# Kernel optimization log

Hardware: AMD Instinct MI355X
Metric: run time of the kernel (lower is better)

The kernel has to match this reference:

```python
import jax, jax.numpy as jnp
import numpy as np

DIM = 2048
HEADS = 16
B = 2
T = 2048


def setup_inputs() -> dict:
    key = jax.random.key(0)
    k_x, k_qkv, k_out, k_b = jax.random.split(key, 4)
    inv = DIM ** -0.5
    return {
        "x": jax.random.normal(k_x, (B, T, DIM), dtype=jnp.float32),
        "w_qkv": jax.random.normal(k_qkv, (DIM, 3 * DIM), dtype=jnp.float32) * inv,
        "w_out": jax.random.normal(k_out, (DIM, DIM), dtype=jnp.float32) * inv,
        "b_out": jnp.zeros((DIM,), dtype=jnp.float32),
    }


def reference(x, w_qkv, w_out, b_out):
    b, t, e = x.shape
    h = HEADS
    d = e // h
    scale = d ** -0.5
    qkv = x @ w_qkv                              # [b, t, 3e]
    q, k, v = jnp.split(qkv, 3, axis=-1)
    # [b, t, e] -> [b, h, t, d]
    q, k, v = (a.reshape(b, t, h, d).transpose(0, 2, 1, 3) for a in (q, k, v))
    dots = jnp.einsum("bhid,bhjd->bhij", q, k) * scale  # [b, h, t, t]
    causal_mask = jnp.triu(jnp.ones((t, t), dtype=bool), k=1)  # True where j > i
    dots = jnp.where(causal_mask[None, None, :, :], -jnp.inf, dots)
    attn = jax.nn.softmax(dots, axis=-1)
    out = jnp.einsum("bhij,bhjd->bhid", attn, v)  # [b, h, t, d]
    out = out.transpose(0, 2, 1, 3).reshape(b, t, e)
    return out @ w_out + b_out
```

## Files before the change

### kernel.cpp

```cpp
#include <hip/hip_runtime.h>
#include <stdint.h>

#define BATCH 2
#define TDIM 2048
#define EDIM 2048
#define NH 16
#define HD 128
#define E3 6144
#define MROWS 4096
#define QKS 4096

typedef short v8bf __attribute__((ext_vector_type(8)));
typedef float v4f  __attribute__((ext_vector_type(4)));

typedef __attribute__((address_space(3))) uint8_t lds_u8;
typedef __attribute__((address_space(1))) uint8_t glb_u8;

__device__ __forceinline__ void gload16(const void* g, void* l) {
    __builtin_amdgcn_global_load_lds((const glb_u8*)g, (lds_u8*)l, 16, 0, 0);
}

__device__ __forceinline__ ushort f2bf(float f) {
    uint32_t u = __float_as_uint(f);
    return (ushort)((u + 0x7fffu + ((u >> 16) & 1u)) >> 16);
}

__device__ __forceinline__ void tcvt_body(const float* __restrict__ in, ushort* __restrict__ out,
                                          int R, int C, int tcb, int trb, int tid) {
    __shared__ float t[32][33];
    const int tc = tcb * 32, tr = trb * 32;
    const int row = tid >> 3, c4 = (tid & 7) * 4;
    const float4 v = *reinterpret_cast<const float4*>(in + (size_t)(tr + row) * C + tc + c4);
    t[row][c4] = v.x; t[row][c4 + 1] = v.y; t[row][c4 + 2] = v.z; t[row][c4 + 3] = v.w;
    __syncthreads();
    const int oc = tid >> 3, r4 = (tid & 7) * 4;
    ushort4 o = make_ushort4(f2bf(t[r4][oc]), f2bf(t[r4 + 1][oc]),
                             f2bf(t[r4 + 2][oc]), f2bf(t[r4 + 3][oc]));
    *reinterpret_cast<ushort4*>(out + (size_t)(tc + oc) * R + tr + r4) = o;
}

#define NB_T1 12288
#define NB_T2 4096
#define NB_CV 2048

__global__ void prep_kernel(const float* __restrict__ x, const float* __restrict__ w_qkv,
                            const float* __restrict__ w_out, ushort* __restrict__ xb,
                            ushort* __restrict__ wqkvT, ushort* __restrict__ woutT) {
    const int bid = blockIdx.x;
    const int tid = threadIdx.x;
    if (bid < NB_T1) {
        tcvt_body(w_qkv, wqkvT, EDIM, E3, bid % (E3 / 32), bid / (E3 / 32), tid);
    } else if (bid < NB_T1 + NB_T2) {
        const int b2 = bid - NB_T1;
        tcvt_body(w_out, woutT, EDIM, EDIM, b2 % (EDIM / 32), b2 / (EDIM / 32), tid);
    } else {
        const int b3 = bid - NB_T1 - NB_T2;
        int i = (b3 * 256 + tid) * 4;
        const int stride = NB_CV * 256 * 4;
        const int n = MROWS * EDIM;
        for (; i < n; i += stride) {
            const float4 v = *reinterpret_cast<const float4*>(x + i);
            ushort4 o = make_ushort4(f2bf(v.x), f2bf(v.y), f2bf(v.z), f2bf(v.w));
            *reinterpret_cast<ushort4*>(xb + i) = o;
        }
    }
}

template <int MODE>
__global__ void gemm_kernel(const ushort* __restrict__ A, const ushort* __restrict__ Bt,
                            void* __restrict__ Cv, const float* __restrict__ bias,
                            ushort* __restrict__ vtout,
                            int Mdim, int Ndim, int Kdim) {
    __shared__ __align__(16) ushort As[128 * 64];
    __shared__ __align__(16) ushort Bs[128 * 64];
    const int tid = threadIdx.x;
    const int lane = tid & 63;
    const int wv = tid >> 6;
    const int l4 = lane >> 4, l16 = lane & 15;
    const int nbn = Ndim >> 7;
    const int nwg = (Mdim >> 7) * nbn;
    int bid = blockIdx.x;
    bid = (bid & 7) * (nwg >> 3) + (bid >> 3);
    const int bm = bid / nbn, bn = bid % nbn;
    const int wr = wv >> 1, wc = wv & 1;

    const ushort* Abase = A + (size_t)(bm * 128) * Kdim;
    const ushort* Bbase = Bt + (size_t)(bn * 128) * Kdim;

    v4f acc[4][4] = {};

    for (int k0 = 0; k0 < Kdim; k0 += 64) {
#pragma unroll
        for (int i = 0; i < 4; ++i) {
            const int c = i * 256 + tid;
            const int row = c >> 3;
            const int kc = (c & 7) ^ (row & 7);
            gload16(Abase + (size_t)row * Kdim + k0 + kc * 8, &As[(i * 256 + wv * 64) * 8]);
        }
#pragma unroll
        for (int i = 0; i < 4; ++i) {
            const int c = i * 256 + tid;
            const int row = c >> 3;
            const int kc = (c & 7) ^ (row & 7);
            gload16(Bbase + (size_t)row * Kdim + k0 + kc * 8, &Bs[(i * 256 + wv * 64) * 8]);
        }
        __syncthreads();
#pragma unroll
        for (int kk = 0; kk < 2; ++kk) {
            v8bf af[4], bfr[4];
#pragma unroll
            for (int m = 0; m < 4; ++m) {
                const int r = wr * 64 + m * 16 + l16;
                const int slot = (kk * 4 + l4) ^ (r & 7);
                af[m] = *reinterpret_cast<const v8bf*>(&As[r * 64 + slot * 8]);
            }
#pragma unroll
            for (int n = 0; n < 4; ++n) {
                const int r = wc * 64 + n * 16 + l16;
                const int slot = (kk * 4 + l4) ^ (r & 7);
                bfr[n] = *reinterpret_cast<const v8bf*>(&Bs[r * 64 + slot * 8]);
            }
#pragma unroll
            for (int m = 0; m < 4; ++m)
#pragma unroll
                for (int n = 0; n < 4; ++n)
                    acc[m][n] = __builtin_amdgcn_mfma_f32_16x16x32_bf16(af[m], bfr[n], acc[m][n], 0, 0, 0);
        }
        __syncthreads();
    }

    const int r0 = bm * 128 + wr * 64 + l4 * 4;
    const int c0 = bn * 128 + wc * 64 + l16;
    if (MODE == 1) {
        float* Cf = (float*)Cv;
#pragma unroll
        for (int n = 0; n < 4; ++n) {
            const float bv = bias[c0 + n * 16];
#pragma unroll
            for (int m = 0; m < 4; ++m)
#pragma unroll
                for (int j = 0; j < 4; ++j)
                    Cf[(size_t)(r0 + m * 16 + j) * Ndim + c0 + n * 16] = acc[m][n][j] + bv;
        }
    } else if (MODE == 2 && bn >= 32) {
        const int h = bn - 32;
#pragma unroll
        for (int m = 0; m < 4; ++m) {
            const int r = r0 + m * 16;
            const int b = r >> 11, t0 = r & 2047;
#pragma unroll
            for (int n = 0; n < 4; ++n) {
                const int dcol = wc * 64 + n * 16 + l16;
                ushort* vp = vtout + (size_t)((b * 16 + h) * 128 + dcol) * TDIM + t0;
#pragma unroll
                for (int j = 0; j < 4; ++j)
                    vp[j] = f2bf(acc[m][n][j]);
            }
        }
    } else {
        const int cstride = (MODE == 2) ? QKS : Ndim;
        const float sc = (MODE == 2 && bn < 16) ? 0.08838834764831845f : 1.0f;
        ushort* Cb = (ushort*)Cv;
#pragma unroll
        for (int n = 0; n < 4; ++n)
#pragma unroll
            for (int m = 0; m < 4; ++m)
#pragma unroll
                for (int j = 0; j < 4; ++j)
                    Cb[(size_t)(r0 + m * 16 + j) * cstride + c0 + n * 16] = f2bf(acc[m][n][j] * sc);
    }
}

__global__ __launch_bounds__(256, 2) void flash_kernel(const ushort* __restrict__ qk,
                                                       const ushort* __restrict__ vt,
                                                       ushort* __restrict__ ao) {
    __shared__ __align__(16) ushort Kl[2][64 * 128];
    __shared__ __align__(16) ushort Vl[2][128 * 64];
    __shared__ __align__(16) ushort Pl[128 * 64];

    const int xi = blockIdx.x;
    const int ti = (xi & 1) ? (xi >> 1) : (15 - (xi >> 1));
    const int h = blockIdx.y;
    const int b = blockIdx.z;
    const int tid = threadIdx.x;
    const int lane = tid & 63;
    const int wv = tid >> 6;
    const int l4 = lane >> 4, l16 = lane & 15;

    const int rbs[2]  = {ti * 64 + wv * 16, TDIM - 64 * (ti + 1) + wv * 16};
    const int diag[2] = {ti, 31 - ti};
    const int nkt = 32 - ti;

    v8bf qf[2][4];
#pragma unroll
    for (int mg = 0; mg < 2; ++mg) {
        const ushort* qp = qk + (size_t)(b * TDIM + rbs[mg] + l16) * QKS + h * HD + l4 * 8;
#pragma unroll
        for (int d0 = 0; d0 < 4; ++d0)
            qf[mg][d0] = *reinterpret_cast<const v8bf*>(qp + d0 * 32);
    }

    float mrun[2][4], lrun[2][4];
#pragma unroll
    for (int mg = 0; mg < 2; ++mg)
#pragma unroll
        for (int j = 0; j < 4; ++j) { mrun[mg][j] = -1e30f; lrun[mg][j] = 0.0f; }
    v4f oacc[2][8] = {};

    const ushort* kbase = qk + (size_t)(b * TDIM) * QKS + EDIM + h * HD;
    const ushort* vbase = vt + (size_t)((b * 16 + h) * HD) * TDIM;

#define STAGE(BUF, KT)                                                                        \
    do {                                                                                      \
        _Pragma("unroll") for (int i = 0; i < 4; ++i) {                                       \
            const int c = i * 256 + tid;                                                      \
            const int row = c >> 4;                                                           \
            const int dc = (c & 15) ^ (row & 7);                                              \
            gload16(kbase + (size_t)((KT) * 64 + row) * QKS + dc * 8,                         \
                    &Kl[BUF][(i * 256 + wv * 64) * 8]);                                       \
        }                                                                                     \
        _Pragma("unroll") for (int i = 0; i < 4; ++i) {                                       \
            const int c = i * 256 + tid;                                                      \
            const int row = c >> 3;                                                           \
            const int jc = (c & 7) ^ (row & 7);                                               \
            gload16(vbase + (size_t)row * TDIM + (KT) * 64 + jc * 8,                          \
                    &Vl[BUF][(i * 256 + wv * 64) * 8]);                                       \
        }                                                                                     \
    } while (0)

    STAGE(0, 0);
    __syncthreads();
    int cur = 0;

    for (int kt = 0; kt < nkt; ++kt) {
        if (kt + 1 < nkt) STAGE(cur ^ 1, kt + 1);

        const bool act0 = (kt <= diag[0]);
        const ushort* Kb = &Kl[cur][0];
        const ushort* Vb = &Vl[cur][0];

        v4f s[2][4] = {};
#pragma unroll
        for (int d0 = 0; d0 < 4; ++d0) {
            v8bf kf[4];
#pragma unroll
            for (int kvn = 0; kvn < 4; ++kvn) {
                const int r = kvn * 16 + l16;
                const int slot = (d0 * 4 + l4) ^ (r & 7);
                kf[kvn] = *reinterpret_cast<const v8bf*>(&Kb[r * 128 + slot * 8]);
            }
#pragma unroll
            for (int kvn = 0; kvn < 4; ++kvn) {
                if (act0)
                    s[0][kvn] = __builtin_amdgcn_mfma_f32_16x16x32_bf16(qf[0][d0], kf[kvn], s[0][kvn], 0, 0, 0);
                s[1][kvn] = __builtin_amdgcn_mfma_f32_16x16x32_bf16(qf[1][d0], kf[kvn], s[1][kvn], 0, 0, 0);
            }
        }

#pragma unroll
        for (int mg = 0; mg < 2; ++mg) {
            if (mg == 0 && !act0) continue;

            float sv[4][4];
#pragma unroll
            for (int kvn = 0; kvn < 4; ++kvn)
#pragma unroll
                for (int j = 0; j < 4; ++j)
                    sv[kvn][j] = s[mg][kvn][j];

            if (kt == diag[mg]) {
                const int rg = rbs[mg] + l4 * 4;
#pragma unroll
                for (int kvn = 0; kvn < 4; ++kvn) {
                    const int cg = kt * 64 + kvn * 16 + l16;
#pragma unroll
                    for (int j = 0; j < 4; ++j)
                        if (cg > rg + j) sv[kvn][j] = -__builtin_inff();
                }
            }

            float pm[4], dmax = -1e30f;
#pragma unroll
            for (int j = 0; j < 4; ++j) {
                float m0 = fmaxf(fmaxf(sv[0][j], sv[1][j]), fmaxf(sv[2][j], sv[3][j]));
                m0 = fmaxf(m0, __shfl_xor(m0, 1));
                m0 = fmaxf(m0, __shfl_xor(m0, 2));
                m0 = fmaxf(m0, __shfl_xor(m0, 4));
                m0 = fmaxf(m0, __shfl_xor(m0, 8));
                pm[j] = m0;
                dmax = fmaxf(dmax, m0 - mrun[mg][j]);
            }
            if (!__all(dmax <= 8.0f)) {
                float corr[4];
#pragma unroll
                for (int j = 0; j < 4; ++j) {
                    const float mn = fmaxf(mrun[mg][j], pm[j]);
                    corr[j] = __expf(mrun[mg][j] - mn);
                    mrun[mg][j] = mn;
                    lrun[mg][j] *= corr[j];
                }
#pragma unroll
                for (int n = 0; n < 8; ++n)
#pragma unroll
                    for (int j = 0; j < 4; ++j)
                        oacc[mg][n][j] *= corr[j];
            }

            float p[4][4];
#pragma unroll
            for (int kvn = 0; kvn < 4; ++kvn)
#pragma unroll
                for (int j = 0; j < 4; ++j)
                    p[kvn][j] = __expf(sv[kvn][j] - mrun[mg][j]);
#pragma unroll
            for (int j = 0; j < 4; ++j)
                lrun[mg][j] += p[0][j] + p[1][j] + p[2][j] + p[3][j];

            const int row = wv * 32 + mg * 16 + l4 * 4;
#pragma unroll
            for (int kvn = 0; kvn < 4; ++kvn) {
                const int cc = kvn * 2 + (l16 >> 3);
#pragma unroll
                for (int j = 0; j < 4; ++j) {
                    const int r = row + j;
                    Pl[r * 64 + ((cc ^ (r & 7)) * 8) + (l16 & 7)] = f2bf(p[kvn][j]);
                }
            }
        }

#pragma unroll
        for (int kk = 0; kk < 2; ++kk) {
            v8bf pf[2];
#pragma unroll
            for (int mg = 0; mg < 2; ++mg) {
                if (mg == 0 && !act0) continue;
                const int r = wv * 32 + mg * 16 + l16;
                const int slot = (kk * 4 + l4) ^ (r & 7);
                pf[mg] = *reinterpret_cast<const v8bf*>(&Pl[r * 64 + slot * 8]);
            }
#pragma unroll
            for (int n = 0; n < 8; ++n) {
                const int dr = n * 16 + l16;
                const int slot = (kk * 4 + l4) ^ (dr & 7);
                v8bf vf = *reinterpret_cast<const v8bf*>(&Vb[dr * 64 + slot * 8]);
                if (act0)
                    oacc[0][n] = __builtin_amdgcn_mfma_f32_16x16x32_bf16(pf[0], vf, oacc[0][n], 0, 0, 0);
                oacc[1][n] = __builtin_amdgcn_mfma_f32_16x16x32_bf16(pf[1], vf, oacc[1][n], 0, 0, 0);
            }
        }
        __syncthreads();
        cur ^= 1;
    }
#undef STAGE

#pragma unroll
    for (int mg = 0; mg < 2; ++mg) {
        float inv[4];
#pragma unroll
        for (int j = 0; j < 4; ++j) {
            float l = lrun[mg][j];
            l += __shfl_xor(l, 1);
            l += __shfl_xor(l, 2);
            l += __shfl_xor(l, 4);
            l += __shfl_xor(l, 8);
            inv[j] = 1.0f / l;
        }
        ushort* aop = ao + (size_t)(b * TDIM + rbs[mg] + l4 * 4) * EDIM + h * HD + l16;
#pragma unroll
        for (int n = 0; n < 8; ++n)
#pragma unroll
            for (int j = 0; j < 4; ++j)
                aop[(size_t)j * EDIM + n * 16] = f2bf(oacc[mg][n][j] * inv[j]);
    }
}

extern "C" void kernel_launch(void* const* d_in, const int* in_sizes, int n_in,
                              void* d_out, int out_size, void* d_ws, size_t ws_size,
                              hipStream_t stream) {
    (void)in_sizes; (void)n_in; (void)out_size; (void)ws_size;
    const float* x     = (const float*)d_in[0];
    const float* w_qkv = (const float*)d_in[1];
    const float* w_out = (const float*)d_in[2];
    const float* b_out = (const float*)d_in[3];

    uint8_t* ws = (uint8_t*)d_ws;
    ushort* qk    = (ushort*)(ws);
    ushort* vtb   = (ushort*)(ws + 33554432u);
    ushort* woutT = (ushort*)(ws + 50331648u);
    ushort* xb    = (ushort*)(ws + 58720256u);
    ushort* wqkvT = (ushort*)(ws + 75497472u);
    ushort* ao    = wqkvT;

    prep_kernel<<<NB_T1 + NB_T2 + NB_CV, 256, 0, stream>>>(x, w_qkv, w_out, xb, wqkvT, woutT);

    gemm_kernel<2><<<(MROWS / 128) * (E3 / 128), 256, 0, stream>>>(
        xb, wqkvT, (void*)qk, nullptr, vtb, MROWS, E3, EDIM);

    flash_kernel<<<dim3(16, NH, BATCH), 256, 0, stream>>>(qk, vtb, ao);

    gemm_kernel<1><<<(MROWS / 128) * (EDIM / 128), 256, 0, stream>>>(
        ao, woutT, d_out, b_out, nullptr, MROWS, EDIM, EDIM);
}
```

Measured before the change: 256.5 us.

## Compute transposed scores and pass P through registers instead of LDS

Swaps the MFMA operand order so each lane holds one query row's scores, which makes the row max and sum mostly lane-local and needs only two cross-lane shuffles. The P matrix is packed to bf16 in registers and rearranged into the A-operand layout with lane shuffles, removing the LDS round trip and its shared buffer. The log2(e) factor is folded into the Q scale at projection time so exp2f can replace __expf. The cost is extra shuffle and select instructions, and a trickier per-row correction broadcast.

```diff
diff --git a/kernel.cpp b/kernel.cpp
--- a/kernel.cpp
+++ b/kernel.cpp
@@ -159,7 +159,8 @@
         }
     } else {
         const int cstride = (MODE == 2) ? QKS : Ndim;
-        const float sc = (MODE == 2 && bn < 16) ? 0.08838834764831845f : 1.0f;
+        const float sc = (MODE == 2 && bn < 16)
+                             ? (0.08838834764831845f * 1.4426950408889634f) : 1.0f;
         ushort* Cb = (ushort*)Cv;
 #pragma unroll
         for (int n = 0; n < 4; ++n)
@@ -176,7 +177,6 @@
                                                        ushort* __restrict__ ao) {
     __shared__ __align__(16) ushort Kl[2][64 * 128];
     __shared__ __align__(16) ushort Vl[2][128 * 64];
-    __shared__ __align__(16) ushort Pl[128 * 64];
 
     const int xi = blockIdx.x;
     const int ti = (xi & 1) ? (xi >> 1) : (15 - (xi >> 1));
@@ -200,11 +200,9 @@
             qf[mg][d0] = *reinterpret_cast<const v8bf*>(qp + d0 * 32);
     }
 
-    float mrun[2][4], lrun[2][4];
-#pragma unroll
-    for (int mg = 0; mg < 2; ++mg)
-#pragma unroll
-        for (int j = 0; j < 4; ++j) { mrun[mg][j] = -1e30f; lrun[mg][j] = 0.0f; }
+    float mrun[2], lrun[2];
+#pragma unroll
+    for (int mg = 0; mg < 2; ++mg) { mrun[mg] = -1e30f; lrun[mg] = 0.0f; }
     v4f oacc[2][8] = {};
 
     const ushort* kbase = qk + (size_t)(b * TDIM) * QKS + EDIM + h * HD;
@@ -252,11 +250,12 @@
 #pragma unroll
             for (int kvn = 0; kvn < 4; ++kvn) {
                 if (act0)
-                    s[0][kvn] = __builtin_amdgcn_mfma_f32_16x16x32_bf16(qf[0][d0], kf[kvn], s[0][kvn], 0, 0, 0);
-                s[1][kvn] = __builtin_amdgcn_mfma_f32_16x16x32_bf16(qf[1][d0], kf[kvn], s[1][kvn], 0, 0, 0);
-            }
-        }
-
+                    s[0][kvn] = __builtin_amdgcn_mfma_f32_16x16x32_bf16(kf[kvn], qf[0][d0], s[0][kvn], 0, 0, 0);
+                s[1][kvn] = __builtin_amdgcn_mfma_f32_16x16x32_bf16(kf[kvn], qf[1][d0], s[1][kvn], 0, 0, 0);
+            }
+        }
+
+        v8bf pf[2][2];
 #pragma unroll
         for (int mg = 0; mg < 2; ++mg) {
             if (mg == 0 && !act0) continue;
@@ -269,83 +268,93 @@
                     sv[kvn][j] = s[mg][kvn][j];
 
             if (kt == diag[mg]) {
-                const int rg = rbs[mg] + l4 * 4;
+                const int qg = rbs[mg] + l16;
 #pragma unroll
                 for (int kvn = 0; kvn < 4; ++kvn) {
-                    const int cg = kt * 64 + kvn * 16 + l16;
+                    const int kvg = kt * 64 + kvn * 16 + l4 * 4;
 #pragma unroll
                     for (int j = 0; j < 4; ++j)
-                        if (cg > rg + j) sv[kvn][j] = -__builtin_inff();
+                        if (kvg + j > qg) sv[kvn][j] = -__builtin_inff();
                 }
             }
 
-            float pm[4], dmax = -1e30f;
-#pragma unroll
-            for (int j = 0; j < 4; ++j) {
-                float m0 = fmaxf(fmaxf(sv[0][j], sv[1][j]), fmaxf(sv[2][j], sv[3][j]));
-                m0 = fmaxf(m0, __shfl_xor(m0, 1));
-                m0 = fmaxf(m0, __shfl_xor(m0, 2));
-                m0 = fmaxf(m0, __shfl_xor(m0, 4));
-                m0 = fmaxf(m0, __shfl_xor(m0, 8));
-                pm[j] = m0;
-                dmax = fmaxf(dmax, m0 - mrun[mg][j]);
-            }
-            if (!__all(dmax <= 8.0f)) {
-                float corr[4];
+            float m0 = sv[0][0];
+#pragma unroll
+            for (int kvn = 0; kvn < 4; ++kvn)
+#pragma unroll
+                for (int j = 0; j < 4; ++j)
+                    m0 = fmaxf(m0, sv[kvn][j]);
+            m0 = fmaxf(m0, __shfl_xor(m0, 16));
+            m0 = fmaxf(m0, __shfl_xor(m0, 32));
+
+            if (!__all(m0 - mrun[mg] <= 8.0f)) {
+                const float mn = fmaxf(mrun[mg], m0);
+                const float corr = exp2f(mrun[mg] - mn);
+                mrun[mg] = mn;
+                lrun[mg] *= corr;
+                float corrj[4];
+#pragma unroll
+                for (int j = 0; j < 4; ++j)
+                    corrj[j] = __shfl(corr, l4 * 4 + j);
+#pragma unroll
+                for (int n = 0; n < 8; ++n)
+#pragma unroll
+                    for (int j = 0; j < 4; ++j)
+                        oacc[mg][n][j] *= corrj[j];
+            }
+
+            float p[4][4], rs = 0.0f;
+#pragma unroll
+            for (int kvn = 0; kvn < 4; ++kvn)
 #pragma unroll
                 for (int j = 0; j < 4; ++j) {
-                    const float mn = fmaxf(mrun[mg][j], pm[j]);
-                    corr[j] = __expf(mrun[mg][j] - mn);
-                    mrun[mg][j] = mn;
-                    lrun[mg][j] *= corr[j];
+                    p[kvn][j] = exp2f(sv[kvn][j] - mrun[mg]);
+                    rs += p[kvn][j];
                 }
-#pragma unroll
-                for (int n = 0; n < 8; ++n)
-#pragma unroll
-                    for (int j = 0; j < 4; ++j)
-                        oacc[mg][n][j] *= corr[j];
-            }
-
-            float p[4][4];
-#pragma unroll
-            for (int kvn = 0; kvn < 4; ++kvn)
-#pragma unroll
-                for (int j = 0; j < 4; ++j)
-                    p[kvn][j] = __expf(sv[kvn][j] - mrun[mg][j]);
-#pragma unroll
-            for (int j = 0; j < 4; ++j)
-                lrun[mg][j] += p[0][j] + p[1][j] + p[2][j] + p[3][j];
-
-            const int row = wv * 32 + mg * 16 + l4 * 4;
+            rs += __shfl_xor(rs, 16);
+            rs += __shfl_xor(rs, 32);
+            lrun[mg] += rs;
+
+            uint32_t wp[4][2];
 #pragma unroll
             for (int kvn = 0; kvn < 4; ++kvn) {
-                const int cc = kvn * 2 + (l16 >> 3);
-#pragma unroll
-                for (int j = 0; j < 4; ++j) {
-                    const int r = row + j;
-                    Pl[r * 64 + ((cc ^ (r & 7)) * 8) + (l16 & 7)] = f2bf(p[kvn][j]);
-                }
+                wp[kvn][0] = (uint32_t)f2bf(p[kvn][0]) | ((uint32_t)f2bf(p[kvn][1]) << 16);
+                wp[kvn][1] = (uint32_t)f2bf(p[kvn][2]) | ((uint32_t)f2bf(p[kvn][3]) << 16);
+            }
+
+            const int srcA = 32 * (l4 & 1) + l16;
+            const int srcB = srcA + 16;
+            const bool hi = (l4 >> 1) != 0;
+#pragma unroll
+            for (int kk = 0; kk < 2; ++kk) {
+                const uint32_t a00 = __shfl(wp[2 * kk][0], srcA);
+                const uint32_t a01 = __shfl(wp[2 * kk][1], srcA);
+                const uint32_t a10 = __shfl(wp[2 * kk + 1][0], srcA);
+                const uint32_t a11 = __shfl(wp[2 * kk + 1][1], srcA);
+                const uint32_t b00 = __shfl(wp[2 * kk][0], srcB);
+                const uint32_t b01 = __shfl(wp[2 * kk][1], srcB);
+                const uint32_t b10 = __shfl(wp[2 * kk + 1][0], srcB);
+                const uint32_t b11 = __shfl(wp[2 * kk + 1][1], srcB);
+                uint32_t w0 = hi ? a10 : a00;
+                uint32_t w1 = hi ? a11 : a01;
+                uint32_t w2 = hi ? b10 : b00;
+                uint32_t w3 = hi ? b11 : b01;
+                union { uint32_t u[4]; v8bf v; } cvt;
+                cvt.u[0] = w0; cvt.u[1] = w1; cvt.u[2] = w2; cvt.u[3] = w3;
+                pf[mg][kk] = cvt.v;
             }
         }
 
 #pragma unroll
         for (int kk = 0; kk < 2; ++kk) {
-            v8bf pf[2];
-#pragma unroll
-            for (int mg = 0; mg < 2; ++mg) {
-                if (mg == 0 && !act0) continue;
-                const int r = wv * 32 + mg * 16 + l16;
-                const int slot = (kk * 4 + l4) ^ (r & 7);
-                pf[mg] = *reinterpret_cast<const v8bf*>(&Pl[r * 64 + slot * 8]);
-            }
 #pragma unroll
             for (int n = 0; n < 8; ++n) {
                 const int dr = n * 16 + l16;
                 const int slot = (kk * 4 + l4) ^ (dr & 7);
                 v8bf vf = *reinterpret_cast<const v8bf*>(&Vb[dr * 64 + slot * 8]);
                 if (act0)
-                    oacc[0][n] = __builtin_amdgcn_mfma_f32_16x16x32_bf16(pf[0], vf, oacc[0][n], 0, 0, 0);
-                oacc[1][n] = __builtin_amdgcn_mfma_f32_16x16x32_bf16(pf[1], vf, oacc[1][n], 0, 0, 0);
+                    oacc[0][n] = __builtin_amdgcn_mfma_f32_16x16x32_bf16(pf[0][kk], vf, oacc[0][n], 0, 0, 0);
+                oacc[1][n] = __builtin_amdgcn_mfma_f32_16x16x32_bf16(pf[1][kk], vf, oacc[1][n], 0, 0, 0);
             }
         }
         __syncthreads();
@@ -355,22 +364,16 @@
 
 #pragma unroll
     for (int mg = 0; mg < 2; ++mg) {
-        float inv[4];
-#pragma unroll
-        for (int j = 0; j < 4; ++j) {
-            float l = lrun[mg][j];
-            l += __shfl_xor(l, 1);
-            l += __shfl_xor(l, 2);
-            l += __shfl_xor(l, 4);
-            l += __shfl_xor(l, 8);
-            inv[j] = 1.0f / l;
-        }
+        float invj[4];
+#pragma unroll
+        for (int j = 0; j < 4; ++j)
+            invj[j] = 1.0f / __shfl(lrun[mg], l4 * 4 + j);
         ushort* aop = ao + (size_t)(b * TDIM + rbs[mg] + l4 * 4) * EDIM + h * HD + l16;
 #pragma unroll
         for (int n = 0; n < 8; ++n)
 #pragma unroll
             for (int j = 0; j < 4; ++j)
-                aop[(size_t)j * EDIM + n * 16] = f2bf(oacc[mg][n][j] * inv[j]);
+                aop[(size_t)j * EDIM + n * 16] = f2bf(oacc[mg][n][j] * invj[j]);
     }
 }
 
```

After: 257.3 us. About the same (+0.3%).
